# Kernel tuning notes

Measured on AMD Instinct MI355X. Metric: run time of the kernel, lower is better.

Reference implementation:

```python
import jax, jax.numpy as jnp
import numpy as np

N_NODES = 50000


def setup_inputs() -> dict:
    key = jax.random.key(0)
    k1, k2, k3, k4, k5 = jax.random.split(key, 5)
    x = jax.random.normal(k1, (N_NODES, 128), dtype=jnp.float32)
    edge_index = jax.random.randint(k2, (2, 800000), 0, N_NODES, dtype=jnp.int64)
    # Linear layers: torch Linear stores weight as [out, in]; init ~ U(-1/sqrt(in), 1/sqrt(in))
    s = 1.0 / np.sqrt(128.0)
    W_rel = jax.random.uniform(k3, (128, 128), dtype=jnp.float32, minval=-s, maxval=s)
    b_rel = jax.random.uniform(k4, (128,), dtype=jnp.float32, minval=-s, maxval=s)
    W_root = jax.random.uniform(k5, (128, 128), dtype=jnp.float32, minval=-s, maxval=s)
    return {"x": x, "edge_index": edge_index, "W_rel": W_rel, "b_rel": b_rel, "W_root": W_root}


def reference(x, edge_index, W_rel, b_rel, W_root):
    # GraphConv (PyG): out_i = W_rel @ (sum_{j -> i} x_j) + b_rel + W_root @ x_i
    src, dst = edge_index[0], edge_index[1]
    msgs = x[src]  # [E, in] gather
    agg = jax.ops.segment_sum(msgs, dst, num_segments=N_NODES)  # [N, in] scatter-add
    out = agg @ W_rel.T + b_rel + x @ W_root.T
    # ReLU; dropout_rate = DropoutRate.NONE -> p=0, identity
    return jax.nn.relu(out)
```

## Files before the change

### kernel.cpp

```cpp
#include <hip/hip_runtime.h>
#include <hip/hip_bf16.h>


#define F 128
#define NPB 32
#define NPARTS 8
#define CAP 128
#define CAPB 768
#define AST 68

typedef __bf16 bf16x8 __attribute__((ext_vector_type(8)));
typedef float f32x4 __attribute__((ext_vector_type(4)));

__device__ inline unsigned f32_to_bf16_rne(float f) {
  unsigned u = __float_as_uint(f);
  unsigned r = u + 0x7fffu + ((u >> 16) & 1u);
  return r >> 16;
}
__device__ inline unsigned pack2(float2 v) {
  return f32_to_bf16_rne(v.x) | (f32_to_bf16_rne(v.y) << 16);
}
__device__ inline void upk(unsigned v, float& ax, float& ay) {
  ax += __uint_as_float(v << 16);
  ay += __uint_as_float(v & 0xffff0000u);
}

__global__ __launch_bounds__(256) void prep_bin_kernel(
    const float2* __restrict__ x, const float2* __restrict__ w0,
    const float2* __restrict__ w1, const int* __restrict__ ei,
    unsigned* __restrict__ xb, unsigned* __restrict__ wb,
    int* __restrict__ binCursor, unsigned* __restrict__ bin,
    int E, int NB, int n2x, int n2w) {
  const int tid0 = blockIdx.x * blockDim.x + threadIdx.x;
  const int stride = gridDim.x * blockDim.x;

  const int totalc = n2x + 2 * n2w;
  for (int i = tid0; i < totalc; i += stride) {
    if (i < n2x) {
      xb[i] = pack2(x[i]);
    } else if (i < n2x + n2w) {
      int j = i - n2x;
      wb[j] = pack2(w0[j]);
    } else {
      int j = i - n2x - n2w;
      wb[n2w + j] = pack2(w1[j]);
    }
  }

  const int part = blockIdx.x & (NPARTS - 1);
  for (int e = tid0; e < E; e += stride) {
    unsigned src = (unsigned)ei[e];
    unsigned dst = (unsigned)ei[E + e];
    unsigned key = (dst << 16) | src;
    int cell = part * NB + (int)(dst >> 5);
    int slot = atomicAdd(&binCursor[cell], 1);
    if (slot < CAP) bin[(size_t)cell * CAP + slot] = key;
  }
}

__global__ __launch_bounds__(512) void agg_gemm_kernel(
    const unsigned* __restrict__ xb, const unsigned* __restrict__ bin,
    const int* __restrict__ binCursor, const __bf16* __restrict__ wb,
    const float* __restrict__ brel, float* __restrict__ out, int N, int NB) {
  __shared__ int cntS[NPB];
  __shared__ int offS[NPB];
  __shared__ int curS[NPB];
  __shared__ unsigned short eLds[CAPB];
  __shared__ unsigned aLds[NPB * AST];
  const int b = blockIdx.x;
  const int t = threadIdx.x;

  if (t < NPB) cntS[t] = 0;
  __syncthreads();

  unsigned kreg[NPARTS];
  int cnt_p[NPARTS];
#pragma unroll
  for (int p = 0; p < NPARTS; ++p) {
    int cell = p * NB + b;
    int c = min(binCursor[cell], CAP);
    cnt_p[p] = c;
    if (t < c) {
      kreg[p] = bin[(size_t)cell * CAP + t];
      atomicAdd(&cntS[(kreg[p] >> 16) & (NPB - 1)], 1);
    }
  }
  __syncthreads();

  if (t < 64) {
    int v = (t < NPB) ? cntS[t] : 0;
    int incl = v;
#pragma unroll
    for (int off = 1; off < NPB; off <<= 1) {
      int u = __shfl_up(incl, off);
      if (t >= off) incl += u;
    }
    if (t < NPB) {
      offS[t] = incl - v;
      curS[t] = incl - v;
    }
  }
  __syncthreads();

#pragma unroll
  for (int p = 0; p < NPARTS; ++p) {
    if (t < cnt_p[p]) {
      int d = (kreg[p] >> 16) & (NPB - 1);
      int pos = atomicAdd(&curS[d], 1);
      if (pos < CAPB) eLds[pos] = (unsigned short)(kreg[p] & 0xffffu);
    }
  }
  __syncthreads();

  const int wave = t >> 6;
  const int lane = t & 63;
  const int nodeBase = b * NPB;
#pragma unroll
  for (int di = wave; di < NPB; di += 8) {
    float ax = 0.f, ay = 0.f;
    int beg = min(offS[di], CAPB);
    int end = min(offS[di] + cntS[di], CAPB);
    int e = beg;
    for (; e + 7 < end; e += 8) {
      int s0 = eLds[e + 0];
      int s1 = eLds[e + 1];
      int s2 = eLds[e + 2];
      int s3 = eLds[e + 3];
      int s4 = eLds[e + 4];
      int s5 = eLds[e + 5];
      int s6 = eLds[e + 6];
      int s7 = eLds[e + 7];
      unsigned v0 = xb[(size_t)s0 * 64 + lane];
      unsigned v1 = xb[(size_t)s1 * 64 + lane];
      unsigned v2 = xb[(size_t)s2 * 64 + lane];
      unsigned v3 = xb[(size_t)s3 * 64 + lane];
      unsigned v4 = xb[(size_t)s4 * 64 + lane];
      unsigned v5 = xb[(size_t)s5 * 64 + lane];
      unsigned v6 = xb[(size_t)s6 * 64 + lane];
      unsigned v7 = xb[(size_t)s7 * 64 + lane];
      upk(v0, ax, ay);
      upk(v1, ax, ay);
      upk(v2, ax, ay);
      upk(v3, ax, ay);
      upk(v4, ax, ay);
      upk(v5, ax, ay);
      upk(v6, ax, ay);
      upk(v7, ax, ay);
    }
    for (; e + 3 < end; e += 4) {
      int s0 = eLds[e + 0];
      int s1 = eLds[e + 1];
      int s2 = eLds[e + 2];
      int s3 = eLds[e + 3];
      unsigned v0 = xb[(size_t)s0 * 64 + lane];
      unsigned v1 = xb[(size_t)s1 * 64 + lane];
      unsigned v2 = xb[(size_t)s2 * 64 + lane];
      unsigned v3 = xb[(size_t)s3 * 64 + lane];
      upk(v0, ax, ay);
      upk(v1, ax, ay);
      upk(v2, ax, ay);
      upk(v3, ax, ay);
    }
    for (; e < end; ++e) upk(xb[(size_t)eLds[e] * 64 + lane], ax, ay);
    aLds[di * AST + lane] = f32_to_bf16_rne(ax) | (f32_to_bf16_rne(ay) << 16);
  }
  __syncthreads();

  const int m16 = lane & 15;
  const int quad = lane >> 4;
  const f32x4 zero4 = {0.f, 0.f, 0.f, 0.f};
  const bf16x8 zero8 = {};
  f32x4 acc[2];
  acc[0] = zero4;
  acc[1] = zero4;

#pragma unroll
  for (int ph = 0; ph < 2; ++ph) {
    const __bf16* __restrict__ W = wb + (size_t)ph * F * F;
#pragma unroll
    for (int k0 = 0; k0 < F; k0 += 32) {
      const int kcol = k0 + 8 * quad;
      bf16x8 a[2], bw;
#pragma unroll
      for (int mt = 0; mt < 2; ++mt) {
        if (ph == 0) {
          a[mt] = *(const bf16x8*)&aLds[(mt * 16 + m16) * AST + (kcol >> 1)];
        } else {
          int row = nodeBase + mt * 16 + m16;
          a[mt] = (row < N)
                      ? *(const bf16x8*)((const __bf16*)xb + (size_t)row * F + kcol)
                      : zero8;
        }
      }
      bw = *(const bf16x8*)(W + (size_t)(wave * 16 + m16) * F + kcol);
#pragma unroll
      for (int mt = 0; mt < 2; ++mt)
        acc[mt] = __builtin_amdgcn_mfma_f32_16x16x32_bf16(a[mt], bw, acc[mt], 0, 0, 0);
    }
  }

  float bias = brel[wave * 16 + m16];
#pragma unroll
  for (int mt = 0; mt < 2; ++mt) {
    int row0 = nodeBase + mt * 16 + quad * 4;
#pragma unroll
    for (int r = 0; r < 4; ++r) {
      int row = row0 + r;
      if (row < N)
        out[(size_t)row * F + wave * 16 + m16] = fmaxf(acc[mt][r] + bias, 0.f);
    }
  }
}

__global__ __launch_bounds__(256) void scatter_add_kernel(
    const float4* __restrict__ x4, const int* __restrict__ ei,
    float* __restrict__ agg, int E) {
  int gid = blockIdx.x * blockDim.x + threadIdx.x;
  if (gid >= E * 32) return;
  int e = gid >> 5, q = gid & 31;
  float4 v = x4[(size_t)ei[e] * 32 + q];
  float* a = agg + (size_t)ei[E + e] * F + q * 4;
  atomicAdd(a + 0, v.x);
  atomicAdd(a + 1, v.y);
  atomicAdd(a + 2, v.z);
  atomicAdd(a + 3, v.w);
}

#define ROWS_PER_BLOCK 64
#define SA_STRIDE 36
#define SW_STRIDE 132

__global__ __launch_bounds__(256) void gemm_fused_kernel(
    const float* __restrict__ agg, const float* __restrict__ x,
    const float* __restrict__ Wrel, const float* __restrict__ Wroot,
    const float* __restrict__ brel, float* __restrict__ out, int N) {
  __shared__ float sA[ROWS_PER_BLOCK * SA_STRIDE];
  __shared__ float sW[32 * SW_STRIDE];
  const int tid = threadIdx.x;
  const int j0 = (tid & 31) * 4;
  const int r0 = (tid >> 5) * 8;
  const int rowBase = blockIdx.x * ROWS_PER_BLOCK;
  float acc[8][4];
#pragma unroll
  for (int r = 0; r < 8; ++r)
#pragma unroll
    for (int c = 0; c < 4; ++c) acc[r][c] = 0.0f;
  for (int phase = 0; phase < 2; ++phase) {
    const float* __restrict__ A = phase ? x : agg;
    const float* __restrict__ W = phase ? Wroot : Wrel;
    for (int kc = 0; kc < F; kc += 32) {
#pragma unroll
      for (int idx = tid; idx < 512; idx += 256) {
        int row = idx >> 3, k4 = idx & 7;
        float4 v = make_float4(0.f, 0.f, 0.f, 0.f);
        int grow = rowBase + row;
        if (grow < N) v = *(const float4*)&A[(size_t)grow * F + kc + k4 * 4];
        *(float4*)&sA[row * SA_STRIDE + k4 * 4] = v;
      }
#pragma unroll
      for (int idx = tid; idx < 4096; idx += 256) {
        int j = idx >> 5, kk = idx & 31;
        sW[kk * SW_STRIDE + j] = W[j * F + kc + kk];
      }
      __syncthreads();
#pragma unroll
      for (int kk = 0; kk < 32; ++kk) {
        float4 w = *(const float4*)&sW[kk * SW_STRIDE + j0];
#pragma unroll
        for (int r = 0; r < 8; ++r) {
          float a = sA[(r0 + r) * SA_STRIDE + kk];
          acc[r][0] = fmaf(a, w.x, acc[r][0]);
          acc[r][1] = fmaf(a, w.y, acc[r][1]);
          acc[r][2] = fmaf(a, w.z, acc[r][2]);
          acc[r][3] = fmaf(a, w.w, acc[r][3]);
        }
      }
      __syncthreads();
    }
  }
  float b0 = brel[j0], b1 = brel[j0 + 1], b2 = brel[j0 + 2], b3 = brel[j0 + 3];
#pragma unroll
  for (int r = 0; r < 8; ++r) {
    int row = rowBase + r0 + r;
    if (row < N) {
      float4 v;
      v.x = fmaxf(acc[r][0] + b0, 0.0f);
      v.y = fmaxf(acc[r][1] + b1, 0.0f);
      v.z = fmaxf(acc[r][2] + b2, 0.0f);
      v.w = fmaxf(acc[r][3] + b3, 0.0f);
      *(float4*)&out[(size_t)row * F + j0] = v;
    }
  }
}

extern "C" void kernel_launch(void* const* d_in, const int* in_sizes, int n_in,
                              void* d_out, int out_size, void* d_ws, size_t ws_size,
                              hipStream_t stream) {
  const float* x     = (const float*)d_in[0];
  const int*   ei    = (const int*)d_in[1];
  const float* Wrel  = (const float*)d_in[2];
  const float* brel  = (const float*)d_in[3];
  const float* Wroot = (const float*)d_in[4];
  float* out = (float*)d_out;

  const int N = in_sizes[0] / F;
  const int E = in_sizes[1] / 2;
  const int NB = (N + NPB - 1) / NPB;

  size_t xbBytes  = ((size_t)N * F * 2 + 255) & ~(size_t)255;
  size_t wBytes   = ((size_t)2 * F * F * 2 + 255) & ~(size_t)255;
  size_t curBytes = ((size_t)NPARTS * NB * sizeof(int) + 255) & ~(size_t)255;
  size_t binBytes = ((size_t)NPARTS * NB * CAP * sizeof(unsigned) + 255) & ~(size_t)255;
  size_t needBin  = curBytes + binBytes + xbBytes + wBytes;

  if (ws_size >= needBin) {
    int*      binCursor = (int*)d_ws;
    unsigned* bin = (unsigned*)((char*)d_ws + curBytes);
    unsigned* xb  = (unsigned*)((char*)d_ws + curBytes + binBytes);
    unsigned* wb  = (unsigned*)((char*)d_ws + curBytes + binBytes + xbBytes);

    const int n2x = N * (F / 2);
    const int n2w = F * F / 2;
    hipMemsetAsync(binCursor, 0, (size_t)NPARTS * NB * sizeof(int), stream);
    prep_bin_kernel<<<2048, 256, 0, stream>>>(
        (const float2*)x, (const float2*)Wrel, (const float2*)Wroot, ei, xb, wb,
        binCursor, bin, E, NB, n2x, n2w);
    agg_gemm_kernel<<<NB, 512, 0, stream>>>(xb, bin, binCursor,
                                            (const __bf16*)wb, brel, out, N, NB);
  } else {
    hipMemsetAsync(out, 0, (size_t)N * F * sizeof(float), stream);
    long long total = (long long)E * 32;
    scatter_add_kernel<<<(int)((total + 255) / 256), 256, 0, stream>>>(
        (const float4*)x, ei, out, E);
    gemm_fused_kernel<<<(N + ROWS_PER_BLOCK - 1) / ROWS_PER_BLOCK, 256, 0,
                        stream>>>(out, x, Wrel, Wroot, brel, out, N);
  }
}
```

Before: 180.4 us.

## Fuse memset, prep/binning and aggregation-GEMM into one cooperative kernel

Replaces the memset plus two-kernel pipeline with a single cooperative kernel launched with one block per 32-node bin. It zeroes the cursors, converts x and the weights to bf16, bins edges, and then does the gather and MFMA GEMM, with grid-wide syncs between phases. Blocks shrink from 512 to 256 threads, so each wave now computes two 16-column output tiles and handles twice as many destination nodes. The 8-way unrolled gather loop is dropped. A fallback to the separate kernels remains if the occupancy check or the cooperative launch fails. This removes launch gaps, but it adds grid-barrier cost and gives each block less gather parallelism.

Result: faster. 169.3 us (-6.1%).

```diff
diff --git a/kernel.cpp b/kernel.cpp
--- a/kernel.cpp
+++ b/kernel.cpp
@@ -1,5 +1,8 @@
 #include <hip/hip_runtime.h>
 #include <hip/hip_bf16.h>
+#include <hip/hip_cooperative_groups.h>
+
+namespace cg = cooperative_groups;
 
 
 #define F 128
@@ -25,50 +28,40 @@
   ay += __uint_as_float(v & 0xffff0000u);
 }
 
-__global__ __launch_bounds__(256) void prep_bin_kernel(
+__global__ __launch_bounds__(256) void mega_kernel(
     const float2* __restrict__ x, const float2* __restrict__ w0,
     const float2* __restrict__ w1, const int* __restrict__ ei,
     unsigned* __restrict__ xb, unsigned* __restrict__ wb,
     int* __restrict__ binCursor, unsigned* __restrict__ bin,
-    int E, int NB, int n2x, int n2w) {
-  const int tid0 = blockIdx.x * blockDim.x + threadIdx.x;
-  const int stride = gridDim.x * blockDim.x;
-
-  const int totalc = n2x + 2 * n2w;
-  for (int i = tid0; i < totalc; i += stride) {
-    if (i < n2x) {
-      xb[i] = pack2(x[i]);
-    } else if (i < n2x + n2w) {
-      int j = i - n2x;
-      wb[j] = pack2(w0[j]);
-    } else {
-      int j = i - n2x - n2w;
-      wb[n2w + j] = pack2(w1[j]);
-    }
-  }
-
-  const int part = blockIdx.x & (NPARTS - 1);
-  for (int e = tid0; e < E; e += stride) {
+    const float* __restrict__ brel, float* __restrict__ out,
+    int N, int E, int NB, int n2x, int n2w) {
+  cg::grid_group grid = cg::this_grid();
+  const int t = threadIdx.x;
+  const int b = blockIdx.x;
+  const int gtid = b * 256 + t;
+  const int gstride = gridDim.x * 256;
+
+  for (int i = gtid; i < NPARTS * NB; i += gstride) binCursor[i] = 0;
+  for (int i = gtid; i < n2x; i += gstride) xb[i] = pack2(x[i]);
+  for (int i = gtid; i < 2 * n2w; i += gstride)
+    wb[i] = (i < n2w) ? pack2(w0[i]) : pack2(w1[i - n2w]);
+  grid.sync();
+
+  const int part = b & (NPARTS - 1);
+  for (int e = gtid; e < E; e += gstride) {
     unsigned src = (unsigned)ei[e];
     unsigned dst = (unsigned)ei[E + e];
-    unsigned key = (dst << 16) | src;
     int cell = part * NB + (int)(dst >> 5);
     int slot = atomicAdd(&binCursor[cell], 1);
-    if (slot < CAP) bin[(size_t)cell * CAP + slot] = key;
-  }
-}
-
-__global__ __launch_bounds__(512) void agg_gemm_kernel(
-    const unsigned* __restrict__ xb, const unsigned* __restrict__ bin,
-    const int* __restrict__ binCursor, const __bf16* __restrict__ wb,
-    const float* __restrict__ brel, float* __restrict__ out, int N, int NB) {
+    if (slot < CAP) bin[(size_t)cell * CAP + slot] = (dst << 16) | src;
+  }
+  grid.sync();
+
   __shared__ int cntS[NPB];
   __shared__ int offS[NPB];
   __shared__ int curS[NPB];
   __shared__ unsigned short eLds[CAPB];
   __shared__ unsigned aLds[NPB * AST];
-  const int b = blockIdx.x;
-  const int t = threadIdx.x;
 
   if (t < NPB) cntS[t] = 0;
   __syncthreads();
@@ -116,37 +109,11 @@
   const int lane = t & 63;
   const int nodeBase = b * NPB;
 #pragma unroll
-  for (int di = wave; di < NPB; di += 8) {
+  for (int di = wave; di < NPB; di += 4) {
     float ax = 0.f, ay = 0.f;
     int beg = min(offS[di], CAPB);
     int end = min(offS[di] + cntS[di], CAPB);
     int e = beg;
-    for (; e + 7 < end; e += 8) {
-      int s0 = eLds[e + 0];
-      int s1 = eLds[e + 1];
-      int s2 = eLds[e + 2];
-      int s3 = eLds[e + 3];
-      int s4 = eLds[e + 4];
-      int s5 = eLds[e + 5];
-      int s6 = eLds[e + 6];
-      int s7 = eLds[e + 7];
-      unsigned v0 = xb[(size_t)s0 * 64 + lane];
-      unsigned v1 = xb[(size_t)s1 * 64 + lane];
-      unsigned v2 = xb[(size_t)s2 * 64 + lane];
-      unsigned v3 = xb[(size_t)s3 * 64 + lane];
-      unsigned v4 = xb[(size_t)s4 * 64 + lane];
-      unsigned v5 = xb[(size_t)s5 * 64 + lane];
-      unsigned v6 = xb[(size_t)s6 * 64 + lane];
-      unsigned v7 = xb[(size_t)s7 * 64 + lane];
-      upk(v0, ax, ay);
-      upk(v1, ax, ay);
-      upk(v2, ax, ay);
-      upk(v3, ax, ay);
-      upk(v4, ax, ay);
-      upk(v5, ax, ay);
-      upk(v6, ax, ay);
-      upk(v7, ax, ay);
-    }
     for (; e + 3 < end; e += 4) {
       int s0 = eLds[e + 0];
       int s1 = eLds[e + 1];
@@ -170,17 +137,20 @@
   const int quad = lane >> 4;
   const f32x4 zero4 = {0.f, 0.f, 0.f, 0.f};
   const bf16x8 zero8 = {};
-  f32x4 acc[2];
-  acc[0] = zero4;
-  acc[1] = zero4;
-
+  f32x4 acc[2][2];
+#pragma unroll
+  for (int mt = 0; mt < 2; ++mt)
+#pragma unroll
+    for (int s = 0; s < 2; ++s) acc[mt][s] = zero4;
+
+  const __bf16* __restrict__ wbb = (const __bf16*)wb;
 #pragma unroll
   for (int ph = 0; ph < 2; ++ph) {
-    const __bf16* __restrict__ W = wb + (size_t)ph * F * F;
+    const __bf16* __restrict__ W = wbb + (size_t)ph * F * F;
 #pragma unroll
     for (int k0 = 0; k0 < F; k0 += 32) {
       const int kcol = k0 + 8 * quad;
-      bf16x8 a[2], bw;
+      bf16x8 a[2], bw[2];
 #pragma unroll
       for (int mt = 0; mt < 2; ++mt) {
         if (ph == 0) {
@@ -192,22 +162,190 @@
                       : zero8;
         }
       }
-      bw = *(const bf16x8*)(W + (size_t)(wave * 16 + m16) * F + kcol);
+#pragma unroll
+      for (int s = 0; s < 2; ++s) {
+        int nt = wave * 2 + s;
+        bw[s] = *(const bf16x8*)(W + (size_t)(nt * 16 + m16) * F + kcol);
+      }
 #pragma unroll
       for (int mt = 0; mt < 2; ++mt)
-        acc[mt] = __builtin_amdgcn_mfma_f32_16x16x32_bf16(a[mt], bw, acc[mt], 0, 0, 0);
-    }
-  }
-
-  float bias = brel[wave * 16 + m16];
-#pragma unroll
-  for (int mt = 0; mt < 2; ++mt) {
-    int row0 = nodeBase + mt * 16 + quad * 4;
-#pragma unroll
-    for (int r = 0; r < 4; ++r) {
-      int row = row0 + r;
-      if (row < N)
-        out[(size_t)row * F + wave * 16 + m16] = fmaxf(acc[mt][r] + bias, 0.f);
+#pragma unroll
+        for (int s = 0; s < 2; ++s)
+          acc[mt][s] = __builtin_amdgcn_mfma_f32_16x16x32_bf16(
+              a[mt], bw[s], acc[mt][s], 0, 0, 0);
+    }
+  }
+
+#pragma unroll
+  for (int s = 0; s < 2; ++s) {
+    int nt = wave * 2 + s;
+    float bias = brel[nt * 16 + m16];
+#pragma unroll
+    for (int mt = 0; mt < 2; ++mt) {
+      int row0 = nodeBase + mt * 16 + quad * 4;
+#pragma unroll
+      for (int r = 0; r < 4; ++r) {
+        int row = row0 + r;
+        if (row < N)
+          out[(size_t)row * F + nt * 16 + m16] = fmaxf(acc[mt][s][r] + bias, 0.f);
+      }
+    }
+  }
+}
+
+__global__ __launch_bounds__(256) void prep_bin_kernel(
+    const float2* __restrict__ x, const float2* __restrict__ w0,
+    const float2* __restrict__ w1, const int* __restrict__ ei,
+    unsigned* __restrict__ xb, unsigned* __restrict__ wb,
+    int* __restrict__ binCursor, unsigned* __restrict__ bin,
+    int E, int NB, int n2x, int n2w) {
+  const int tid0 = blockIdx.x * blockDim.x + threadIdx.x;
+  const int stride = gridDim.x * blockDim.x;
+  const int totalc = n2x + 2 * n2w;
+  for (int i = tid0; i < totalc; i += stride) {
+    if (i < n2x) xb[i] = pack2(x[i]);
+    else if (i < n2x + n2w) wb[i - n2x] = pack2(w0[i - n2x]);
+    else wb[i - n2x] = pack2(w1[i - n2x - n2w]);
+  }
+  const int part = blockIdx.x & (NPARTS - 1);
+  for (int e = tid0; e < E; e += stride) {
+    unsigned src = (unsigned)ei[e];
+    unsigned dst = (unsigned)ei[E + e];
+    int cell = part * NB + (int)(dst >> 5);
+    int slot = atomicAdd(&binCursor[cell], 1);
+    if (slot < CAP) bin[(size_t)cell * CAP + slot] = (dst << 16) | src;
+  }
+}
+
+__global__ __launch_bounds__(256) void agg_gemm_kernel(
+    const unsigned* __restrict__ xb, const unsigned* __restrict__ bin,
+    const int* __restrict__ binCursor, const __bf16* __restrict__ wb,
+    const float* __restrict__ brel, float* __restrict__ out, int N, int NB) {
+  __shared__ int cntS[NPB];
+  __shared__ int offS[NPB];
+  __shared__ int curS[NPB];
+  __shared__ unsigned short eLds[CAPB];
+  __shared__ unsigned aLds[NPB * AST];
+  const int b = blockIdx.x;
+  const int t = threadIdx.x;
+  if (t < NPB) cntS[t] = 0;
+  __syncthreads();
+  unsigned kreg[NPARTS];
+  int cnt_p[NPARTS];
+#pragma unroll
+  for (int p = 0; p < NPARTS; ++p) {
+    int cell = p * NB + b;
+    int c = min(binCursor[cell], CAP);
+    cnt_p[p] = c;
+    if (t < c) {
+      kreg[p] = bin[(size_t)cell * CAP + t];
+      atomicAdd(&cntS[(kreg[p] >> 16) & (NPB - 1)], 1);
+    }
+  }
+  __syncthreads();
+  if (t < 64) {
+    int v = (t < NPB) ? cntS[t] : 0;
+    int incl = v;
+#pragma unroll
+    for (int off = 1; off < NPB; off <<= 1) {
+      int u = __shfl_up(incl, off);
+      if (t >= off) incl += u;
+    }
+    if (t < NPB) {
+      offS[t] = incl - v;
+      curS[t] = incl - v;
+    }
+  }
+  __syncthreads();
+#pragma unroll
+  for (int p = 0; p < NPARTS; ++p) {
+    if (t < cnt_p[p]) {
+      int d = (kreg[p] >> 16) & (NPB - 1);
+      int pos = atomicAdd(&curS[d], 1);
+      if (pos < CAPB) eLds[pos] = (unsigned short)(kreg[p] & 0xffffu);
+    }
+  }
+  __syncthreads();
+  const int wave = t >> 6;
+  const int lane = t & 63;
+  const int nodeBase = b * NPB;
+#pragma unroll
+  for (int di = wave; di < NPB; di += 4) {
+    float ax = 0.f, ay = 0.f;
+    int beg = min(offS[di], CAPB);
+    int end = min(offS[di] + cntS[di], CAPB);
+    int e = beg;
+    for (; e + 3 < end; e += 4) {
+      int s0 = eLds[e + 0];
+      int s1 = eLds[e + 1];
+      int s2 = eLds[e + 2];
+      int s3 = eLds[e + 3];
+      unsigned v0 = xb[(size_t)s0 * 64 + lane];
+      unsigned v1 = xb[(size_t)s1 * 64 + lane];
+      unsigned v2 = xb[(size_t)s2 * 64 + lane];
+      unsigned v3 = xb[(size_t)s3 * 64 + lane];
+      upk(v0, ax, ay);
+      upk(v1, ax, ay);
+      upk(v2, ax, ay);
+      upk(v3, ax, ay);
+    }
+    for (; e < end; ++e) upk(xb[(size_t)eLds[e] * 64 + lane], ax, ay);
+    aLds[di * AST + lane] = f32_to_bf16_rne(ax) | (f32_to_bf16_rne(ay) << 16);
+  }
+  __syncthreads();
+  const int m16 = lane & 15;
+  const int quad = lane >> 4;
+  const f32x4 zero4 = {0.f, 0.f, 0.f, 0.f};
+  const bf16x8 zero8 = {};
+  f32x4 acc[2][2];
+#pragma unroll
+  for (int mt = 0; mt < 2; ++mt)
+#pragma unroll
+    for (int s = 0; s < 2; ++s) acc[mt][s] = zero4;
+#pragma unroll
+  for (int ph = 0; ph < 2; ++ph) {
+    const __bf16* __restrict__ W = wb + (size_t)ph * F * F;
+#pragma unroll
+    for (int k0 = 0; k0 < F; k0 += 32) {
+      const int kcol = k0 + 8 * quad;
+      bf16x8 a[2], bw[2];
+#pragma unroll
+      for (int mt = 0; mt < 2; ++mt) {
+        if (ph == 0) {
+          a[mt] = *(const bf16x8*)&aLds[(mt * 16 + m16) * AST + (kcol >> 1)];
+        } else {
+          int row = nodeBase + mt * 16 + m16;
+          a[mt] = (row < N)
+                      ? *(const bf16x8*)((const __bf16*)xb + (size_t)row * F + kcol)
+                      : zero8;
+        }
+      }
+#pragma unroll
+      for (int s = 0; s < 2; ++s) {
+        int nt = wave * 2 + s;
+        bw[s] = *(const bf16x8*)(W + (size_t)(nt * 16 + m16) * F + kcol);
+      }
+#pragma unroll
+      for (int mt = 0; mt < 2; ++mt)
+#pragma unroll
+        for (int s = 0; s < 2; ++s)
+          acc[mt][s] = __builtin_amdgcn_mfma_f32_16x16x32_bf16(
+              a[mt], bw[s], acc[mt][s], 0, 0, 0);
+    }
+  }
+#pragma unroll
+  for (int s = 0; s < 2; ++s) {
+    int nt = wave * 2 + s;
+    float bias = brel[nt * 16 + m16];
+#pragma unroll
+    for (int mt = 0; mt < 2; ++mt) {
+      int row0 = nodeBase + mt * 16 + quad * 4;
+#pragma unroll
+      for (int r = 0; r < 4; ++r) {
+        int row = row0 + r;
+        if (row < N)
+          out[(size_t)row * F + nt * 16 + m16] = fmaxf(acc[mt][s][r] + bias, 0.f);
+      }
     }
   }
 }
@@ -319,13 +457,32 @@
     unsigned* xb  = (unsigned*)((char*)d_ws + curBytes + binBytes);
     unsigned* wb  = (unsigned*)((char*)d_ws + curBytes + binBytes + xbBytes);
 
-    const int n2x = N * (F / 2);
-    const int n2w = F * F / 2;
+    int n2x = N * (F / 2);
+    int n2w = F * F / 2;
+
+    int maxBlocksPerCU = 0;
+    hipError_t qerr = hipOccupancyMaxActiveBlocksPerMultiprocessor(
+        &maxBlocksPerCU, (const void*)mega_kernel, 256, 0);
+    bool coopOk = (qerr == hipSuccess) && (maxBlocksPerCU * 256 >= NB);
+
+    if (coopOk) {
+      const float2* xa = (const float2*)x;
+      const float2* w0 = (const float2*)Wrel;
+      const float2* w1 = (const float2*)Wroot;
+      void* args[] = {(void*)&xa, (void*)&w0, (void*)&w1, (void*)&ei,
+                      (void*)&xb, (void*)&wb, (void*)&binCursor, (void*)&bin,
+                      (void*)&brel, (void*)&out,
+                      (void*)&N, (void*)&E, (void*)&NB, (void*)&n2x, (void*)&n2w};
+      hipError_t lerr = hipLaunchCooperativeKernel(
+          (const void*)mega_kernel, dim3(NB), dim3(256), args, 0, stream);
+      if (lerr == hipSuccess) return;
+    }
+
     hipMemsetAsync(binCursor, 0, (size_t)NPARTS * NB * sizeof(int), stream);
     prep_bin_kernel<<<2048, 256, 0, stream>>>(
         (const float2*)x, (const float2*)Wrel, (const float2*)Wroot, ei, xb, wb,
         binCursor, bin, E, NB, n2x, n2w);
-    agg_gemm_kernel<<<NB, 512, 0, stream>>>(xb, bin, binCursor,
+    agg_gemm_kernel<<<NB, 256, 0, stream>>>(xb, bin, binCursor,
                                             (const __bf16*)wb, brel, out, N, NB);
   } else {
     hipMemsetAsync(out, 0, (size_t)N * F * sizeof(float), stream);
```
